# Optimization experiments

Measured on AMD Instinct MI355X. Metric: run time of the kernel, lower is better.

## Reference

```python
import jax, jax.numpy as jnp
import numpy as np

N = 50000
E = 800000
IN_DIM = 512
H1 = IN_DIM // 2   # 256
H2 = IN_DIM // 4   # 128
D = 8
NP_CAYLEY = D * (D - 1) // 2  # 28


def setup_inputs() -> dict:
    key = jax.random.key(0)
    ks = jax.random.split(key, 10)
    x = jax.random.normal(ks[0], (N, IN_DIM), dtype=jnp.float32)
    edge_index = jax.random.randint(ks[1], (2, E), 0, N, dtype=jnp.int64)
    s1 = 1.0 / np.sqrt(IN_DIM)
    s2 = 1.0 / np.sqrt(H1)
    s3 = 1.0 / np.sqrt(H2)
    W1l = jax.random.uniform(ks[2], (H1, IN_DIM), jnp.float32, -s1, s1)
    b1 = jax.random.uniform(ks[3], (H1,), jnp.float32, -s1, s1)
    W1r = jax.random.uniform(ks[4], (H1, IN_DIM), jnp.float32, -s1, s1)
    W2l = jax.random.uniform(ks[5], (H2, H1), jnp.float32, -s2, s2)
    b2 = jax.random.uniform(ks[6], (H2,), jnp.float32, -s2, s2)
    W2r = jax.random.uniform(ks[7], (H2, H1), jnp.float32, -s2, s2)
    Wp = jax.random.uniform(ks[8], (NP_CAYLEY, H2), jnp.float32, -s3, s3)
    bp = jax.random.uniform(ks[9], (NP_CAYLEY,), jnp.float32, -s3, s3)
    return {"x": x, "edge_index": edge_index,
            "W1l": W1l, "b1": b1, "W1r": W1r,
            "W2l": W2l, "b2": b2, "W2r": W2r,
            "Wp": Wp, "bp": bp}


def _sage_conv(x, src, dst, Wl, bl, Wr):
    # PyG SAGEConv (mean aggr): out = lin_l(mean_{j in N(i)} x_j) + lin_r(x_i)
    msg_sum = jax.ops.segment_sum(x[src], dst, num_segments=N)  # [N, F]
    deg = jax.ops.segment_sum(jnp.ones((src.shape[0],), x.dtype), dst,
                              num_segments=N)
    mean = msg_sum / jnp.maximum(deg, 1.0)[:, None]
    return mean @ Wl.T + bl + x @ Wr.T


def _cayley(params):
    # params: [N, d(d-1)/2] -> skew A, then O = (I - A)^{-1} (I + A)
    iu, ju = jnp.triu_indices(D, k=1)  # row-major i<j matches torch loop order
    n = params.shape[0]
    A = jnp.zeros((n, D, D), params.dtype)
    A = A.at[:, iu, ju].set(params)
    A = A.at[:, ju, iu].set(-params)
    I = jnp.eye(D, dtype=params.dtype)
    return jnp.linalg.solve(I[None] - A, I[None] + A)


def reference(x, edge_index, W1l, b1, W1r, W2l, b2, W2r, Wp, bp):
    src, dst = edge_index[0], edge_index[1]
    h = jax.nn.relu(_sage_conv(x, src, dst, W1l, b1, W1r))
    h = jax.nn.relu(_sage_conv(h, src, dst, W2l, b2, W2r))
    params = h @ Wp.T + bp  # [N, 28]
    return _cayley(params)  # [N, 8, 8]
```

## Files before the change

### kernel.cpp

```cpp
#include <hip/hip_runtime.h>
#include <hip/hip_bf16.h>


#define WS_ALIGN(x) (((x) + 255) & ~size_t(255))

typedef __attribute__((ext_vector_type(8))) short short8;
typedef __attribute__((ext_vector_type(4))) float floatx4;

static __device__ __forceinline__ ushort f2b(float f) {
    unsigned u = __builtin_bit_cast(unsigned, f);
    u = (u + 0x7fffu + ((u >> 16) & 1u)) >> 16;
    return (ushort)u;
}
static __device__ __forceinline__ float b2f(ushort h) {
    unsigned u = ((unsigned)h) << 16;
    return __builtin_bit_cast(float, u);
}
static __device__ __forceinline__ unsigned pk2(float a, float b) {
    return (unsigned)f2b(a) | ((unsigned)f2b(b) << 16);
}


__global__ void hist_kernel(const int* __restrict__ dst, int* __restrict__ deg, int E) {
    int e = blockIdx.x * blockDim.x + threadIdx.x;
    if (e < E) atomicAdd(&deg[dst[e]], 1);
}

__global__ __launch_bounds__(256)
void scan_phase1(const int* __restrict__ deg, int* __restrict__ bsum, int n) {
    __shared__ int red[256];
    const int t = threadIdx.x;
    const int i = blockIdx.x * 1024 + t * 4;
    int s = 0;
    if (i + 4 <= n) {
        int4 v = *reinterpret_cast<const int4*>(&deg[i]);
        s = v.x + v.y + v.z + v.w;
    } else {
        for (int k = i; k < n; ++k) s += deg[k];
    }
    red[t] = s;
    __syncthreads();
#pragma unroll
    for (int off = 128; off > 0; off >>= 1) {
        if (t < off) red[t] += red[t + off];
        __syncthreads();
    }
    if (t == 0) bsum[blockIdx.x] = red[0];
}

__global__ __launch_bounds__(256)
void scan_phase2(int* __restrict__ bsum, int* __restrict__ rowptr, int nb, int n) {
    __shared__ int sh[256];
    const int t = threadIdx.x;
    int orig = (t < nb) ? bsum[t] : 0;
    sh[t] = orig;
    __syncthreads();
#pragma unroll
    for (int off = 1; off < 256; off <<= 1) {
        int v = (t >= off) ? sh[t - off] : 0;
        __syncthreads();
        sh[t] += v;
        __syncthreads();
    }
    if (t < nb) bsum[t] = sh[t] - orig;
    if (t == 255) rowptr[n] = sh[255];
}

__global__ __launch_bounds__(256)
void scan_phase3(const int* __restrict__ deg, const int* __restrict__ bsum,
                 int* __restrict__ rowptr, int n) {
    __shared__ int red[256];
    const int t = threadIdx.x;
    const int i = blockIdx.x * 1024 + t * 4;
    int v0 = 0, v1 = 0, v2 = 0, v3 = 0;
    if (i + 4 <= n) {
        int4 v = *reinterpret_cast<const int4*>(&deg[i]);
        v0 = v.x; v1 = v.y; v2 = v.z; v3 = v.w;
    } else {
        if (i     < n) v0 = deg[i];
        if (i + 1 < n) v1 = deg[i + 1];
        if (i + 2 < n) v2 = deg[i + 2];
        if (i + 3 < n) v3 = deg[i + 3];
    }
    int s = v0 + v1 + v2 + v3;
    red[t] = s;
    __syncthreads();
#pragma unroll
    for (int off = 1; off < 256; off <<= 1) {
        int u = (t >= off) ? red[t - off] : 0;
        __syncthreads();
        red[t] += u;
        __syncthreads();
    }
    int pre = bsum[blockIdx.x] + red[t] - s;
    if (i + 4 <= n) {
        int4 o;
        o.x = pre; o.y = pre + v0; o.z = pre + v0 + v1; o.w = pre + v0 + v1 + v2;
        *reinterpret_cast<int4*>(&rowptr[i]) = o;
    } else {
        if (i     < n) rowptr[i]     = pre;
        if (i + 1 < n) rowptr[i + 1] = pre + v0;
        if (i + 2 < n) rowptr[i + 2] = pre + v0 + v1;
        if (i + 3 < n) rowptr[i + 3] = pre + v0 + v1 + v2;
    }
}

__global__ void scatter_kernel(const int* __restrict__ src, const int* __restrict__ dst,
                               const int* __restrict__ rowptr, int* __restrict__ cursor,
                               int* __restrict__ adj, int E) {
    int e = blockIdx.x * blockDim.x + threadIdx.x;
    if (e < E) {
        int d = dst[e];
        int p = atomicAdd(&cursor[d], 1);
        adj[rowptr[d] + p] = src[e];
    }
}

__global__ void build_wcat(const float* __restrict__ W1l, const float* __restrict__ W1r,
                           const float* __restrict__ W2l, const float* __restrict__ W2r,
                           ushort* __restrict__ Wc1, ushort* __restrict__ Wc2) {
    int idx = blockIdx.x * blockDim.x + threadIdx.x;
    const int n1 = (512 * 512) / 8;
    const int n2 = (256 * 256) / 8;
    const float* src;
    ushort* dst;
    if (idx < n1) {
        int e = idx * 8;
        int row = e >> 9, col = e & 511;
        src = (row < 256) ? &W1l[row * 512 + col] : &W1r[(row - 256) * 512 + col];
        dst = &Wc1[e];
    } else if (idx < n1 + n2) {
        int e = (idx - n1) * 8;
        int row = e >> 8, col = e & 255;
        src = (row < 128) ? &W2l[row * 256 + col] : &W2r[(row - 128) * 256 + col];
        dst = &Wc2[e];
    } else {
        return;
    }
    const float4* s4 = reinterpret_cast<const float4*>(src);
    float4 v0 = s4[0], v1 = s4[1];
    short8 o;
    o[0] = (short)f2b(v0.x); o[1] = (short)f2b(v0.y);
    o[2] = (short)f2b(v0.z); o[3] = (short)f2b(v0.w);
    o[4] = (short)f2b(v1.x); o[5] = (short)f2b(v1.y);
    o[6] = (short)f2b(v1.z); o[7] = (short)f2b(v1.w);
    *reinterpret_cast<short8*>(dst) = o;
}


template <bool CASTA>
__global__ __launch_bounds__(256, 2)
void gemm_wide(const float* __restrict__ Af, const ushort* __restrict__ Ab,
               const ushort* __restrict__ B,
               ushort* __restrict__ Cl, ushort* __restrict__ Cr,
               int M, int K, int Ncols, int S) {
    __shared__ ushort As[128 * 64];
    __shared__ ushort Bs[256 * 64];
    const int tid  = threadIdx.x;
    const int wave = tid >> 6;
    const int lane = tid & 63;
    const int row0 = blockIdx.y * 128;
    const int col0 = blockIdx.x * 256;
    const int wm = (wave & 1) * 64;
    const int wn = (wave >> 1) * 128;

    floatx4 acc[4][8];
#pragma unroll
    for (int i = 0; i < 4; ++i)
#pragma unroll
        for (int j = 0; j < 8; ++j)
            acc[i][j] = (floatx4){0.f, 0.f, 0.f, 0.f};

    const int rsub = lane >> 3;
    const int ksw  = ((lane & 7) * 16) ^ (rsub << 4);

    for (int k0 = 0; k0 < K; k0 += 64) {
        if constexpr (CASTA) {
            const int r = tid >> 1, h = tid & 1;
            int grow = row0 + r; if (grow >= M) grow = M - 1;
            const float* srow = Af + (size_t)grow * K + k0 + h * 32;
            char* lrow = (char*)As + r * 128;
            const int rx = (r & 7) << 4;
#pragma unroll
            for (int half = 0; half < 2; ++half) {
                float4 v0 = *reinterpret_cast<const float4*>(srow + half * 16 + 0);
                float4 v1 = *reinterpret_cast<const float4*>(srow + half * 16 + 4);
                float4 v2 = *reinterpret_cast<const float4*>(srow + half * 16 + 8);
                float4 v3 = *reinterpret_cast<const float4*>(srow + half * 16 + 12);
                int g0 = h * 4 + half * 2;
                uint4 o0 = make_uint4(pk2(v0.x, v0.y), pk2(v0.z, v0.w),
                                      pk2(v1.x, v1.y), pk2(v1.z, v1.w));
                uint4 o1 = make_uint4(pk2(v2.x, v2.y), pk2(v2.z, v2.w),
                                      pk2(v3.x, v3.y), pk2(v3.z, v3.w));
                *reinterpret_cast<uint4*>(lrow + ((g0 * 16) ^ rx))       = o0;
                *reinterpret_cast<uint4*>(lrow + (((g0 + 1) * 16) ^ rx)) = o1;
            }
        } else {
#pragma unroll
            for (int i = 0; i < 4; ++i) {
                int chunk = wave * 4 + i;
                int r = chunk * 8 + rsub;
                int grow = row0 + r;
                if (grow >= M) grow = M - 1;
                const char* src = (const char*)(Ab + (size_t)grow * K + k0) + ksw;
                __builtin_amdgcn_global_load_lds(
                    (const __attribute__((address_space(1))) unsigned int*)src,
                    (__attribute__((address_space(3))) unsigned int*)(&As[chunk * 512]),
                    16, 0, 0);
            }
        }
#pragma unroll
        for (int i = 0; i < 8; ++i) {
            int chunk = wave * 8 + i;
            int r = chunk * 8 + rsub;
            int gcol = col0 + r;
            const char* src = (const char*)(B + (size_t)gcol * K + k0) + ksw;
            __builtin_amdgcn_global_load_lds(
                (const __attribute__((address_space(1))) unsigned int*)src,
                (__attribute__((address_space(3))) unsigned int*)(&Bs[chunk * 512]),
                16, 0, 0);
        }
        __syncthreads();

#pragma unroll
        for (int kk = 0; kk < 2; ++kk) {
            short8 af[4], bf[8];
            const int kb = (kk * 64 + ((lane >> 4) << 4)) ^ ((lane & 7) << 4);
#pragma unroll
            for (int im = 0; im < 4; ++im) {
                int r = wm + im * 16 + (lane & 15);
                af[im] = *reinterpret_cast<const short8*>((const char*)As + r * 128 + kb);
            }
#pragma unroll
            for (int in = 0; in < 8; ++in) {
                int r = wn + in * 16 + (lane & 15);
                bf[in] = *reinterpret_cast<const short8*>((const char*)Bs + r * 128 + kb);
            }
#pragma unroll
            for (int im = 0; im < 4; ++im)
#pragma unroll
                for (int in = 0; in < 8; ++in)
                    acc[im][in] = __builtin_amdgcn_mfma_f32_16x16x32_bf16(
                        af[im], bf[in], acc[im][in], 0, 0, 0);
        }
        __syncthreads();
    }

#pragma unroll
    for (int im = 0; im < 4; ++im) {
#pragma unroll
        for (int reg = 0; reg < 4; ++reg) {
            int r = row0 + wm + im * 16 + ((lane >> 4) << 2) + reg;
            if (r < M) {
#pragma unroll
                for (int in = 0; in < 8; ++in) {
                    int g = col0 + wn + in * 16 + (lane & 15);
                    if (g < S) Cl[(size_t)r * S + g] = f2b(acc[im][in][reg]);
                    else       Cr[(size_t)r * S + (g - S)] = f2b(acc[im][in][reg]);
                }
            }
        }
    }
}


template <int LPN>
__global__ __launch_bounds__(256)
void aggregate_bf16(const ushort* __restrict__ Yl, const ushort* __restrict__ Yr,
                    const float* __restrict__ bias,
                    const int* __restrict__ rowptr, const int* __restrict__ adj,
                    ushort* __restrict__ H, int n) {
    constexpr int F = LPN * 8;
    const int grp = threadIdx.x / LPN;
    const int sub = threadIdx.x % LPN;
    const int node = blockIdx.x * (256 / LPN) + grp;
    if (node >= n) return;
    const int c = sub * 8;
    const int start = rowptr[node], end = rowptr[node + 1];

    float acc[8];
#pragma unroll
    for (int v = 0; v < 8; ++v) acc[v] = 0.f;

    int e = start;
    for (; e + 4 <= end; e += 4) {
        int s0 = adj[e + 0], s1 = adj[e + 1], s2 = adj[e + 2], s3 = adj[e + 3];
        short8 r0 = *reinterpret_cast<const short8*>(&Yl[(size_t)s0 * F + c]);
        short8 r1 = *reinterpret_cast<const short8*>(&Yl[(size_t)s1 * F + c]);
        short8 r2 = *reinterpret_cast<const short8*>(&Yl[(size_t)s2 * F + c]);
        short8 r3 = *reinterpret_cast<const short8*>(&Yl[(size_t)s3 * F + c]);
#pragma unroll
        for (int v = 0; v < 8; ++v)
            acc[v] += (b2f((ushort)r0[v]) + b2f((ushort)r1[v])) +
                      (b2f((ushort)r2[v]) + b2f((ushort)r3[v]));
    }
    for (; e < end; ++e) {
        int s = adj[e];
        short8 r = *reinterpret_cast<const short8*>(&Yl[(size_t)s * F + c]);
#pragma unroll
        for (int v = 0; v < 8; ++v) acc[v] += b2f((ushort)r[v]);
    }

    const int d = end - start;
    const float inv = 1.0f / (float)(d > 0 ? d : 1);
    short8 sv = *reinterpret_cast<const short8*>(&Yr[(size_t)node * F + c]);
    float4 bv0 = *reinterpret_cast<const float4*>(&bias[c]);
    float4 bv1 = *reinterpret_cast<const float4*>(&bias[c + 4]);
    float bb[8] = {bv0.x, bv0.y, bv0.z, bv0.w, bv1.x, bv1.y, bv1.z, bv1.w};
    short8 o;
#pragma unroll
    for (int v = 0; v < 8; ++v)
        o[v] = (short)f2b(fmaxf(acc[v] * inv + b2f((ushort)sv[v]) + bb[v], 0.f));
    *reinterpret_cast<short8*>(&H[(size_t)node * F + c]) = o;
}


__global__ __launch_bounds__(256)
void params_kernel(const ushort* __restrict__ H2, const float* __restrict__ Wp,
                   const float* __restrict__ bp, float* __restrict__ P, int n) {
    __shared__ float WpS[32 * 132];
    __shared__ float bpS[32];
    for (int t = threadIdx.x; t < 32 * 132; t += 256) WpS[t] = 0.f;
    if (threadIdx.x < 32) bpS[threadIdx.x] = (threadIdx.x < 28) ? bp[threadIdx.x] : 0.f;
    __syncthreads();
    for (int t = threadIdx.x; t < 28 * 128; t += 256) {
        int r = t >> 7, c = t & 127;
        WpS[r * 132 + c] = Wp[t];
    }
    __syncthreads();

    const int node = blockIdx.x * 32 + (threadIdx.x >> 3);
    const int l = threadIdx.x & 7;
    if (node >= n) return;

    short8 h8[16];
    const short8* hp = reinterpret_cast<const short8*>(&H2[(size_t)node * 128]);
#pragma unroll
    for (int q = 0; q < 16; ++q) h8[q] = hp[q];

    float acc0 = bpS[l], acc1 = bpS[l + 8], acc2 = bpS[l + 16], acc3 = bpS[l + 24];
#pragma unroll
    for (int q = 0; q < 32; ++q) {
        float h0 = b2f((ushort)h8[q >> 1][(q & 1) * 4 + 0]);
        float h1 = b2f((ushort)h8[q >> 1][(q & 1) * 4 + 1]);
        float h2 = b2f((ushort)h8[q >> 1][(q & 1) * 4 + 2]);
        float h3 = b2f((ushort)h8[q >> 1][(q & 1) * 4 + 3]);
        float4 w0 = *reinterpret_cast<const float4*>(&WpS[(l +  0) * 132 + 4 * q]);
        float4 w1 = *reinterpret_cast<const float4*>(&WpS[(l +  8) * 132 + 4 * q]);
        float4 w2 = *reinterpret_cast<const float4*>(&WpS[(l + 16) * 132 + 4 * q]);
        float4 w3 = *reinterpret_cast<const float4*>(&WpS[(l + 24) * 132 + 4 * q]);
        acc0 += h0 * w0.x + h1 * w0.y + h2 * w0.z + h3 * w0.w;
        acc1 += h0 * w1.x + h1 * w1.y + h2 * w1.z + h3 * w1.w;
        acc2 += h0 * w2.x + h1 * w2.y + h2 * w2.z + h3 * w2.w;
        acc3 += h0 * w3.x + h1 * w3.y + h2 * w3.z + h3 * w3.w;
    }
    float* pout = &P[(size_t)node * 32];
    pout[l]      = acc0;
    pout[l + 8]  = acc1;
    pout[l + 16] = acc2;
    pout[l + 24] = acc3;
}


__global__ __launch_bounds__(256)
void cayley_kernel(const float* __restrict__ P, float* __restrict__ Out, int n) {
    int i = blockIdx.x * blockDim.x + threadIdx.x;
    if (i >= n) return;
    float p[28];
    const float4* pp = reinterpret_cast<const float4*>(&P[(size_t)i * 32]);
#pragma unroll
    for (int q = 0; q < 7; ++q) {
        float4 v = pp[q];
        p[4 * q + 0] = v.x; p[4 * q + 1] = v.y;
        p[4 * q + 2] = v.z; p[4 * q + 3] = v.w;
    }

    float M_[8][8], B_[8][8];
#pragma unroll
    for (int r = 0; r < 8; ++r)
#pragma unroll
        for (int c = 0; c < 8; ++c) {
            M_[r][c] = (r == c) ? 1.f : 0.f;
            B_[r][c] = (r == c) ? 1.f : 0.f;
        }
    {
        int idx = 0;
#pragma unroll
        for (int r = 0; r < 8; ++r)
#pragma unroll
            for (int c = r + 1; c < 8; ++c) {
                float a = p[idx++];
                M_[r][c] -= a;  M_[c][r] += a;
                B_[r][c] += a;  B_[c][r] -= a;
            }
    }
#pragma unroll
    for (int col = 0; col < 8; ++col) {
        float inv = 1.0f / M_[col][col];
#pragma unroll
        for (int c = 0; c < 8; ++c) { M_[col][c] *= inv; B_[col][c] *= inv; }
#pragma unroll
        for (int r = 0; r < 8; ++r) {
            if (r == col) continue;
            float f = M_[r][col];
#pragma unroll
            for (int c = 0; c < 8; ++c) {
                M_[r][c] -= f * M_[col][c];
                B_[r][c] -= f * B_[col][c];
            }
        }
    }
    float* out = &Out[(size_t)i * 64];
#pragma unroll
    for (int r = 0; r < 8; ++r) {
        float4 o0 = make_float4(B_[r][0], B_[r][1], B_[r][2], B_[r][3]);
        float4 o1 = make_float4(B_[r][4], B_[r][5], B_[r][6], B_[r][7]);
        *reinterpret_cast<float4*>(&out[r * 8 + 0]) = o0;
        *reinterpret_cast<float4*>(&out[r * 8 + 4]) = o1;
    }
}


extern "C" void kernel_launch(void* const* d_in, const int* in_sizes, int n_in,
                              void* d_out, int out_size, void* d_ws, size_t ws_size,
                              hipStream_t stream) {
    const float* x   = (const float*)d_in[0];
    const int*   ei  = (const int*)d_in[1];
    const float* W1l = (const float*)d_in[2];
    const float* b1  = (const float*)d_in[3];
    const float* W1r = (const float*)d_in[4];
    const float* W2l = (const float*)d_in[5];
    const float* b2  = (const float*)d_in[6];
    const float* W2r = (const float*)d_in[7];
    const float* Wp  = (const float*)d_in[8];
    const float* bp  = (const float*)d_in[9];
    float* out = (float*)d_out;

    const int IN_DIM = 512;
    const int N = in_sizes[0] / IN_DIM;
    const int E = in_sizes[1] / 2;

    char* ws = (char*)d_ws;
    size_t off = 0;
    int* deg      = (int*)(ws + off); off = WS_ALIGN(off + (size_t)N * 4);
    int* rowptr   = (int*)(ws + off); off = WS_ALIGN(off + (size_t)(N + 1) * 4);
    int* cursor   = (int*)(ws + off); off = WS_ALIGN(off + (size_t)N * 4);
    int* bsum     = (int*)(ws + off); off = WS_ALIGN(off + (size_t)256 * 4);
    int* adj      = (int*)(ws + off); off = WS_ALIGN(off + (size_t)E * 4);
    ushort* Yl    = (ushort*)(ws + off); off = WS_ALIGN(off + (size_t)N * 256 * 2);
    ushort* Yr    = (ushort*)(ws + off); off = WS_ALIGN(off + (size_t)N * 256 * 2);
    ushort* h1    = (ushort*)(ws + off); off = WS_ALIGN(off + (size_t)N * 256 * 2);
    ushort* zl    = (ushort*)(ws + off); off = WS_ALIGN(off + (size_t)N * 128 * 2);
    ushort* zr    = (ushort*)(ws + off); off = WS_ALIGN(off + (size_t)N * 128 * 2);
    ushort* Wc1   = (ushort*)(ws + off); off = WS_ALIGN(off + (size_t)512 * 512 * 2);
    ushort* Wc2   = (ushort*)(ws + off); off = WS_ALIGN(off + (size_t)256 * 256 * 2);
    float*  Pp    = (float*)(ws + off);  off = WS_ALIGN(off + (size_t)N * 32 * 4);

    const int* src = ei;
    const int* dst = ei + E;

    hipMemsetAsync(deg, 0, (size_t)N * 4, stream);
    hipMemsetAsync(cursor, 0, (size_t)N * 4, stream);

    int eb = (E + 255) / 256;
    int nb = (N + 1023) / 1024;
    hist_kernel<<<eb, 256, 0, stream>>>(dst, deg, E);
    scan_phase1<<<nb, 256, 0, stream>>>(deg, bsum, N);
    scan_phase2<<<1, 256, 0, stream>>>(bsum, rowptr, nb, N);
    scan_phase3<<<nb, 256, 0, stream>>>(deg, bsum, rowptr, N);
    scatter_kernel<<<eb, 256, 0, stream>>>(src, dst, rowptr, cursor, adj, E);

    build_wcat<<<((512 * 512 + 256 * 256) / 8 + 255) / 256, 256, 0, stream>>>(
        W1l, W1r, W2l, W2r, Wc1, Wc2);

    int gm = (N + 127) / 128;

    gemm_wide<true><<<dim3(2, gm), 256, 0, stream>>>(
        x, (const ushort*)nullptr, Wc1, Yl, Yr, N, 512, 512, 256);
    aggregate_bf16<32><<<(N + 7) / 8, 256, 0, stream>>>(Yl, Yr, b1, rowptr, adj, h1, N);

    gemm_wide<false><<<dim3(1, gm), 256, 0, stream>>>(
        (const float*)nullptr, h1, Wc2, zl, zr, N, 256, 256, 128);
    ushort* h2 = Yl;
    aggregate_bf16<16><<<(N + 15) / 16, 256, 0, stream>>>(zl, zr, b2, rowptr, adj, h2, N);

    params_kernel<<<(N + 31) / 32, 256, 0, stream>>>(h2, Wp, bp, Pp, N);
    cayley_kernel<<<(N + 255) / 256, 256, 0, stream>>>(Pp, out, N);
}
```

Measured before the change: 295.4 us.

## Use 8 waves per GEMM block and register-prefetch the fp32 A tile

The wide GEMM now runs 512 threads per block in a 2x4 wave grid, each wave owning a 64x64 sub-tile instead of 64x128. This halves accumulator registers per wave and raises occupancy (launch bounds 512,4). In the cast path, the next K-slice of fp32 A is loaded into registers while the current slice is converted and written to LDS, which hides global latency. The B and A load loops are reassigned across the eight waves. More waves per block means more barrier participants, and each wave does fewer MFMAs per fragment load, so LDS reuse per wave drops.

```diff
diff --git a/kernel.cpp b/kernel.cpp
--- a/kernel.cpp
+++ b/kernel.cpp
@@ -149,7 +149,7 @@
 
 
 template <bool CASTA>
-__global__ __launch_bounds__(256, 2)
+__global__ __launch_bounds__(512, 4)
 void gemm_wide(const float* __restrict__ Af, const ushort* __restrict__ Ab,
                const ushort* __restrict__ B,
                ushort* __restrict__ Cl, ushort* __restrict__ Cr,
@@ -162,43 +162,65 @@
     const int row0 = blockIdx.y * 128;
     const int col0 = blockIdx.x * 256;
     const int wm = (wave & 1) * 64;
-    const int wn = (wave >> 1) * 128;
-
-    floatx4 acc[4][8];
+    const int wn = (wave >> 1) * 64;
+
+    floatx4 acc[4][4];
 #pragma unroll
     for (int i = 0; i < 4; ++i)
 #pragma unroll
-        for (int j = 0; j < 8; ++j)
+        for (int j = 0; j < 4; ++j)
             acc[i][j] = (floatx4){0.f, 0.f, 0.f, 0.f};
 
     const int rsub = lane >> 3;
     const int ksw  = ((lane & 7) * 16) ^ (rsub << 4);
 
+    const int ar = tid >> 2;
+    const int aq = tid & 3;
+    int agrow = row0 + ar; if (agrow >= M) agrow = M - 1;
+    const float* arow_base = CASTA ? (Af + (size_t)agrow * K + aq * 16) : nullptr;
+    char* alds = (char*)As + ar * 128;
+    const int arx = (ar & 7) << 4;
+
+    float4 va0, va1, va2, va3;
+    if constexpr (CASTA) {
+        const float* s0 = arow_base;
+        va0 = *reinterpret_cast<const float4*>(s0 + 0);
+        va1 = *reinterpret_cast<const float4*>(s0 + 4);
+        va2 = *reinterpret_cast<const float4*>(s0 + 8);
+        va3 = *reinterpret_cast<const float4*>(s0 + 12);
+    }
+
     for (int k0 = 0; k0 < K; k0 += 64) {
+#pragma unroll
+        for (int i = 0; i < 4; ++i) {
+            int chunk = wave * 4 + i;
+            int r = chunk * 8 + rsub;
+            int gcol = col0 + r;
+            const char* src = (const char*)(B + (size_t)gcol * K + k0) + ksw;
+            __builtin_amdgcn_global_load_lds(
+                (const __attribute__((address_space(1))) unsigned int*)src,
+                (__attribute__((address_space(3))) unsigned int*)(&Bs[chunk * 512]),
+                16, 0, 0);
+        }
         if constexpr (CASTA) {
-            const int r = tid >> 1, h = tid & 1;
-            int grow = row0 + r; if (grow >= M) grow = M - 1;
-            const float* srow = Af + (size_t)grow * K + k0 + h * 32;
-            char* lrow = (char*)As + r * 128;
-            const int rx = (r & 7) << 4;
-#pragma unroll
-            for (int half = 0; half < 2; ++half) {
-                float4 v0 = *reinterpret_cast<const float4*>(srow + half * 16 + 0);
-                float4 v1 = *reinterpret_cast<const float4*>(srow + half * 16 + 4);
-                float4 v2 = *reinterpret_cast<const float4*>(srow + half * 16 + 8);
-                float4 v3 = *reinterpret_cast<const float4*>(srow + half * 16 + 12);
-                int g0 = h * 4 + half * 2;
-                uint4 o0 = make_uint4(pk2(v0.x, v0.y), pk2(v0.z, v0.w),
-                                      pk2(v1.x, v1.y), pk2(v1.z, v1.w));
-                uint4 o1 = make_uint4(pk2(v2.x, v2.y), pk2(v2.z, v2.w),
-                                      pk2(v3.x, v3.y), pk2(v3.z, v3.w));
-                *reinterpret_cast<uint4*>(lrow + ((g0 * 16) ^ rx))       = o0;
-                *reinterpret_cast<uint4*>(lrow + (((g0 + 1) * 16) ^ rx)) = o1;
+            uint4 o0 = make_uint4(pk2(va0.x, va0.y), pk2(va0.z, va0.w),
+                                  pk2(va1.x, va1.y), pk2(va1.z, va1.w));
+            uint4 o1 = make_uint4(pk2(va2.x, va2.y), pk2(va2.z, va2.w),
+                                  pk2(va3.x, va3.y), pk2(va3.z, va3.w));
+            int g0 = aq * 2;
+            *reinterpret_cast<uint4*>(alds + ((g0 * 16) ^ arx))       = o0;
+            *reinterpret_cast<uint4*>(alds + (((g0 + 1) * 16) ^ arx)) = o1;
+            if (k0 + 64 < K) {
+                const float* s1 = arow_base + k0 + 64;
+                va0 = *reinterpret_cast<const float4*>(s1 + 0);
+                va1 = *reinterpret_cast<const float4*>(s1 + 4);
+                va2 = *reinterpret_cast<const float4*>(s1 + 8);
+                va3 = *reinterpret_cast<const float4*>(s1 + 12);
             }
         } else {
 #pragma unroll
-            for (int i = 0; i < 4; ++i) {
-                int chunk = wave * 4 + i;
+            for (int i = 0; i < 2; ++i) {
+                int chunk = wave * 2 + i;
                 int r = chunk * 8 + rsub;
                 int grow = row0 + r;
                 if (grow >= M) grow = M - 1;
@@ -209,22 +231,11 @@
                     16, 0, 0);
             }
         }
-#pragma unroll
-        for (int i = 0; i < 8; ++i) {
-            int chunk = wave * 8 + i;
-            int r = chunk * 8 + rsub;
-            int gcol = col0 + r;
-            const char* src = (const char*)(B + (size_t)gcol * K + k0) + ksw;
-            __builtin_amdgcn_global_load_lds(
-                (const __attribute__((address_space(1))) unsigned int*)src,
-                (__attribute__((address_space(3))) unsigned int*)(&Bs[chunk * 512]),
-                16, 0, 0);
-        }
         __syncthreads();
 
 #pragma unroll
         for (int kk = 0; kk < 2; ++kk) {
-            short8 af[4], bf[8];
+            short8 af[4], bf[4];
             const int kb = (kk * 64 + ((lane >> 4) << 4)) ^ ((lane & 7) << 4);
 #pragma unroll
             for (int im = 0; im < 4; ++im) {
@@ -232,14 +243,14 @@
                 af[im] = *reinterpret_cast<const short8*>((const char*)As + r * 128 + kb);
             }
 #pragma unroll
-            for (int in = 0; in < 8; ++in) {
+            for (int in = 0; in < 4; ++in) {
                 int r = wn + in * 16 + (lane & 15);
                 bf[in] = *reinterpret_cast<const short8*>((const char*)Bs + r * 128 + kb);
             }
 #pragma unroll
             for (int im = 0; im < 4; ++im)
 #pragma unroll
-                for (int in = 0; in < 8; ++in)
+                for (int in = 0; in < 4; ++in)
                     acc[im][in] = __builtin_amdgcn_mfma_f32_16x16x32_bf16(
                         af[im], bf[in], acc[im][in], 0, 0, 0);
         }
@@ -253,7 +264,7 @@
             int r = row0 + wm + im * 16 + ((lane >> 4) << 2) + reg;
             if (r < M) {
 #pragma unroll
-                for (int in = 0; in < 8; ++in) {
+                for (int in = 0; in < 4; ++in) {
                     int g = col0 + wn + in * 16 + (lane & 15);
                     if (g < S) Cl[(size_t)r * S + g] = f2b(acc[im][in][reg]);
                     else       Cr[(size_t)r * S + (g - S)] = f2b(acc[im][in][reg]);
@@ -475,11 +486,11 @@
 
     int gm = (N + 127) / 128;
 
-    gemm_wide<true><<<dim3(2, gm), 256, 0, stream>>>(
+    gemm_wide<true><<<dim3(2, gm), 512, 0, stream>>>(
         x, (const ushort*)nullptr, Wc1, Yl, Yr, N, 512, 512, 256);
     aggregate_bf16<32><<<(N + 7) / 8, 256, 0, stream>>>(Yl, Yr, b1, rowptr, adj, h1, N);
 
-    gemm_wide<false><<<dim3(1, gm), 256, 0, stream>>>(
+    gemm_wide<false><<<dim3(1, gm), 512, 0, stream>>>(
         (const float*)nullptr, h1, Wc2, zl, zr, N, 256, 256, 128);
     ushort* h2 = Yl;
     aggregate_bf16<16><<<(N + 15) / 16, 256, 0, stream>>>(zl, zr, b2, rowptr, adj, h2, N);
```

Measured after the change: 276.7 us. -6.3%, faster.
